# Kernel tuning notes

Measured on AMD Instinct MI355X. Metric: run time of the kernel, lower is better.

## Reference

```python
import jax, jax.numpy as jnp
import numpy as np

N = 100_000      # nodes
E = 1_600_000    # edges (before self loops)
IN = 128         # in_dim
HID = 64         # hidden_dim (per head)
HEADS = 2
NEG_SLOPE = 0.2  # PyG GATConv default negative_slope


def setup_inputs() -> dict:
    key = jax.random.key(0)
    k = jax.random.split(key, 6)
    x = jax.random.normal(k[0], (N, IN), jnp.float32)
    edge_index = jax.random.randint(k[1], (2, E), 0, N, dtype=jnp.int64)
    # GATConv linear (no bias in lin, bias added after aggregation in PyG)
    W = jax.random.normal(k[2], (IN, HEADS * HID), jnp.float32) * (1.0 / np.sqrt(IN))
    att_src = jax.random.normal(k[3], (HEADS, HID), jnp.float32) * 0.1
    att_dst = jax.random.normal(k[4], (HEADS, HID), jnp.float32) * 0.1
    bias = jnp.zeros((HEADS * HID,), jnp.float32)
    prelu_w = jnp.full((HEADS * HID,), 0.25, jnp.float32)  # nn.PReLU default init
    return {"x": x, "edge_index": edge_index, "W": W, "att_src": att_src,
            "att_dst": att_dst, "bias": bias, "prelu_w": prelu_w}


def reference(x, edge_index, W, att_src, att_dst, bias, prelu_w):
    n = x.shape[0]
    h = (x @ W).reshape(n, HEADS, HID)                 # [N,H,C]
    a_s = jnp.einsum('nhc,hc->nh', h, att_src)         # [N,H]
    a_d = jnp.einsum('nhc,hc->nh', h, att_dst)         # [N,H]
    # add self loops (PyG default add_self_loops=True)
    loops = jnp.arange(n, dtype=edge_index.dtype)
    src = jnp.concatenate([edge_index[0], loops])      # [Et]
    dst = jnp.concatenate([edge_index[1], loops])      # [Et]
    logits = a_s[src] + a_d[dst]                       # [Et,H]
    logits = jnp.where(logits >= 0, logits, NEG_SLOPE * logits)  # LeakyReLU
    # segment softmax over destination neighborhoods
    m = jax.ops.segment_max(logits, dst, num_segments=n)         # [N,H]
    e = jnp.exp(logits - m[dst])
    s = jax.ops.segment_sum(e, dst, num_segments=n)              # [N,H]
    alpha = e / (s[dst] + 1e-16)                                 # [Et,H]
    # (attention dropout p=0.2 is identity in eval mode)
    msg = h[src] * alpha[..., None]                    # [Et,H,C]
    out = jax.ops.segment_sum(msg, dst, num_segments=n).reshape(n, HEADS * HID)
    out = out + bias
    # PReLU with per-channel weight
    return jnp.where(out >= 0, out, prelu_w * out)
```

## Files before the change

### kernel.cpp

```cpp
#include <hip/hip_runtime.h>
#include <hip/hip_fp16.h>
#include <cstdint>
#include <cstddef>

#define NEG_SLOPE 0.2f
#define BSH 9
#define BNODES 512
#define CAP 12288

typedef __attribute__((ext_vector_type(8))) short short8v;
typedef __attribute__((ext_vector_type(4))) float f32x4;

__device__ __forceinline__ uint32_t bf16pair(float a, float b) {
    uint32_t ua = __float_as_uint(a), ub = __float_as_uint(b);
    ua = (ua + 0x7fffu + ((ua >> 16) & 1u)) >> 16;
    ub = (ub + 0x7fffu + ((ub >> 16) & 1u)) >> 16;
    return ua | (ub << 16);
}
__device__ __forceinline__ uint16_t rne16(float f) {
    uint32_t u = __float_as_uint(f);
    return (uint16_t)((u + 0x7fffu + ((u >> 16) & 1u)) >> 16);
}
__device__ __forceinline__ float bflo(uint32_t u) { return __uint_as_float(u << 16); }
__device__ __forceinline__ float bfhi(uint32_t u) { return __uint_as_float(u & 0xffff0000u); }
__device__ __forceinline__ uint32_t packf16(float a, float b) {
    __half2 h = __floats2half2_rn(a, b);
    return *reinterpret_cast<uint32_t*>(&h);
}

__global__ __launch_bounds__(256, 3) void gemm_att(
    const float* __restrict__ x, const float* __restrict__ W,
    const float* __restrict__ att_src, const float* __restrict__ att_dst,
    uint32_t* __restrict__ hb, float* __restrict__ a_s, float* __restrict__ a_d,
    int n)
{
    constexpr int PW = 136;
    __shared__ unsigned short Wt[128 * PW];
    __shared__ unsigned short Hs[4][16 * PW];
    const int tid  = threadIdx.x;
    const int w    = tid >> 6;
    const int lane = tid & 63;
    const int cl   = lane & 15;
    const int gq   = lane >> 4;
    const int base = blockIdx.x * 64;

    const float4* W4 = (const float4*)W;
#pragma unroll
    for (int i = 0; i < 16; ++i) {
        int idx = tid + i * 256;
        int k = idx >> 5, c0 = (idx & 31) * 4;
        float4 v = W4[idx];
        Wt[(c0 + 0) * PW + k] = rne16(v.x);
        Wt[(c0 + 1) * PW + k] = rne16(v.y);
        Wt[(c0 + 2) * PW + k] = rne16(v.z);
        Wt[(c0 + 3) * PW + k] = rne16(v.w);
    }

    float asr[8], adr[8];
#pragma unroll
    for (int t = 0; t < 8; ++t) {
        asr[t] = att_src[t * 16 + cl];
        adr[t] = att_dst[t * 16 + cl];
    }
    __syncthreads();

    const int rowg = base + w * 16 + cl;
    const int rowc = rowg < n ? rowg : (n - 1);
    const float4* xp = (const float4*)(x + (size_t)rowc * 128);

    f32x4 acc[8];
#pragma unroll
    for (int t = 0; t < 8; ++t) acc[t] = (f32x4){0.f, 0.f, 0.f, 0.f};

#pragma unroll
    for (int s = 0; s < 4; ++s) {
        int kq = s * 8 + gq * 2;
        float4 f0 = xp[kq], f1 = xp[kq + 1];
        union { short8v v; uint32_t d[4]; } A;
        A.d[0] = bf16pair(f0.x, f0.y);
        A.d[1] = bf16pair(f0.z, f0.w);
        A.d[2] = bf16pair(f1.x, f1.y);
        A.d[3] = bf16pair(f1.z, f1.w);
#pragma unroll
        for (int t = 0; t < 8; ++t) {
            union { short8v v; uint4 q; } B;
            B.q = *(const uint4*)&Wt[(t * 16 + cl) * PW + s * 32 + gq * 8];
            acc[t] = __builtin_amdgcn_mfma_f32_16x16x32_bf16(A.v, B.v, acc[t], 0, 0, 0);
        }
    }

    float ps0[4], ps1[4], pd0[4], pd1[4];
#pragma unroll
    for (int r = 0; r < 4; ++r) { ps0[r] = ps1[r] = pd0[r] = pd1[r] = 0.f; }
#pragma unroll
    for (int t = 0; t < 8; ++t) {
#pragma unroll
        for (int r = 0; r < 4; ++r) {
            float v = acc[t][r];
            if (t < 4) { ps0[r] = fmaf(v, asr[t], ps0[r]); pd0[r] = fmaf(v, adr[t], pd0[r]); }
            else       { ps1[r] = fmaf(v, asr[t], ps1[r]); pd1[r] = fmaf(v, adr[t], pd1[r]); }
        }
    }
#pragma unroll
    for (int off = 1; off < 16; off <<= 1) {
#pragma unroll
        for (int r = 0; r < 4; ++r) {
            ps0[r] += __shfl_xor(ps0[r], off);
            ps1[r] += __shfl_xor(ps1[r], off);
            pd0[r] += __shfl_xor(pd0[r], off);
            pd1[r] += __shfl_xor(pd1[r], off);
        }
    }
    if (cl == 0) {
#pragma unroll
        for (int r = 0; r < 4; ++r) {
            int rg = base + w * 16 + gq * 4 + r;
            if (rg < n) {
                a_s[rg * 2 + 0] = ps0[r]; a_s[rg * 2 + 1] = ps1[r];
                a_d[rg * 2 + 0] = pd0[r]; a_d[rg * 2 + 1] = pd1[r];
            }
        }
    }

#pragma unroll
    for (int t = 0; t < 8; ++t) {
#pragma unroll
        for (int r = 0; r < 4; ++r) {
            int row = gq * 4 + r;
            Hs[w][row * PW + t * 16 + cl] = rne16(acc[t][r]);
        }
    }
    __syncthreads();
#pragma unroll
    for (int q = 0; q < 4; ++q) {
        int row = q * 4 + gq;
        int cu  = 4 * cl;
        uint4 v = *(const uint4*)&Hs[w][row * PW + cu * 2];
        int rg = base + w * 16 + row;
        if (rg < n) *(uint4*)&hb[(size_t)rg * 64 + cu] = v;
    }
}

__global__ void zero_gcur(int* gcur, int nb) {
    if ((int)threadIdx.x < nb) gcur[threadIdx.x] = 0;
}

__global__ __launch_bounds__(256) void bucket_scatter(
    const int* __restrict__ src, const int* __restrict__ dst,
    int* __restrict__ gcur, uint32_t* __restrict__ pairs, int e, int nb)
{
    __shared__ int histL[256];
    __shared__ int gbaseL[256];
    const int tid = threadIdx.x;
    const int t0  = blockIdx.x * 4096;

    if (tid < nb) histL[tid] = 0;
    __syncthreads();

    int      myb[16];
    int      myslot[16];
    uint32_t mypk[16];
#pragma unroll 16
    for (int k = 0; k < 16; ++k) {
        int i = t0 + tid + k * 256;
        if (i < e) {
            int s = src[i], d = dst[i];
            int b = d >> BSH;
            myb[k]    = b;
            mypk[k]   = (uint32_t)s | ((uint32_t)(d & (BNODES - 1)) << 17);
            myslot[k] = atomicAdd(&histL[b], 1);
        } else myb[k] = -1;
    }
    __syncthreads();
    if (tid < nb) {
        int c = histL[tid];
        gbaseL[tid] = c ? atomicAdd(&gcur[tid], c) : 0;
    }
    __syncthreads();
#pragma unroll 16
    for (int k = 0; k < 16; ++k) {
        if (myb[k] >= 0) {
            int p = gbaseL[myb[k]] + myslot[k];
            if (p < CAP) pairs[(size_t)myb[k] * CAP + p] = mypk[k];
        }
    }
}

__global__ __launch_bounds__(256) void bucket_scan(
    const int* __restrict__ gcur, int* __restrict__ bbase, int* __restrict__ bcnt,
    int nb, int n)
{
    __shared__ int sh[256];
    const int tid = threadIdx.x;
    int nodes = 0, c = 0;
    if (tid < nb) {
        nodes = min(BNODES, n - tid * BNODES);
        c = min(gcur[tid], CAP);
    }
    int tot = c + nodes;
    sh[tid] = tot;
    __syncthreads();
    for (int off = 1; off < 256; off <<= 1) {
        int t = (tid >= off) ? sh[tid - off] : 0;
        __syncthreads();
        sh[tid] += t;
        __syncthreads();
    }
    if (tid < nb) { bbase[tid] = sh[tid] - tot; bcnt[tid] = c; }
}

__global__ __launch_bounds__(512) void build_csr(
    const uint32_t* __restrict__ pairs, const int* __restrict__ bbase,
    const int* __restrict__ bcnt, const float* __restrict__ a_s,
    const float* __restrict__ a_d,
    int* __restrict__ row_ptr, int* __restrict__ cnt, int* __restrict__ col,
    uint32_t* __restrict__ alph, float2* __restrict__ invs, int n)
{
    __shared__ uint32_t pl[CAP];
    __shared__ int degL[BNODES], curL[BNODES], scanL[BNODES];
    __shared__ float sumL[BNODES * 2];
    __shared__ float adL[BNODES * 2];
    const int b = blockIdx.x, tid = threadIdx.x;
    const int nbase = b * BNODES;
    const int nodes = min(BNODES, n - nbase);
    const int C     = bcnt[b];
    const int base  = bbase[b];

    degL[tid] = 1;
    float es0 = 0.f, es1 = 0.f;
    if (tid < nodes) {
        int g = nbase + tid;
        float2 ad = ((const float2*)a_d)[g];
        adL[2 * tid]     = ad.x;
        adL[2 * tid + 1] = ad.y;
        float2 as = ((const float2*)a_s)[g];
        float l0 = as.x + ad.x; l0 = l0 >= 0.f ? l0 : NEG_SLOPE * l0;
        float l1 = as.y + ad.y; l1 = l1 >= 0.f ? l1 : NEG_SLOPE * l1;
        es0 = __expf(l0); es1 = __expf(l1);
        sumL[2 * tid] = es0; sumL[2 * tid + 1] = es1;
    }
    __syncthreads();
    for (int i = tid; i < C; i += 512) {
        uint32_t p = pairs[(size_t)b * CAP + i];
        pl[i] = p;
        atomicAdd(&degL[p >> 17], 1);
    }
    __syncthreads();
    int v = (tid < nodes) ? degL[tid] : 0;
    scanL[tid] = v;
    __syncthreads();
    for (int off = 1; off < 512; off <<= 1) {
        int t = (tid >= off) ? scanL[tid - off] : 0;
        __syncthreads();
        scanL[tid] += t;
        __syncthreads();
    }
    if (tid < nodes) {
        int exc = scanL[tid] - v;
        int g   = nbase + tid;
        row_ptr[g] = base + exc;
        cnt[g]     = v;
        col[base + exc]  = g;
        alph[base + exc] = packf16(es0, es1);
        curL[tid]  = exc + 1;
    }
    __syncthreads();
    for (int i = tid; i < C; i += 512) {
        uint32_t p  = pl[i];
        int dl  = p >> 17;
        int s   = p & 0x1FFFF;
        float2 as = ((const float2*)a_s)[s];
        float l0 = as.x + adL[2 * dl];     l0 = l0 >= 0.f ? l0 : NEG_SLOPE * l0;
        float l1 = as.y + adL[2 * dl + 1]; l1 = l1 >= 0.f ? l1 : NEG_SLOPE * l1;
        float e0 = __expf(l0), e1 = __expf(l1);
        int pos = atomicAdd(&curL[dl], 1);
        col[base + pos]  = s;
        alph[base + pos] = packf16(e0, e1);
        atomicAdd(&sumL[2 * dl],     e0);
        atomicAdd(&sumL[2 * dl + 1], e1);
    }
    __syncthreads();
    if (tid < nodes) {
        float2 iv;
        iv.x = 1.f / (sumL[2 * tid]     + 1e-16f);
        iv.y = 1.f / (sumL[2 * tid + 1] + 1e-16f);
        invs[nbase + tid] = iv;
    }
}

__global__ __launch_bounds__(256) void attn_agg(
    const uint32_t* __restrict__ hb, const uint32_t* __restrict__ alph,
    const float2* __restrict__ invs, const int* __restrict__ row_ptr,
    const int* __restrict__ cnt, const int* __restrict__ col,
    const float* __restrict__ bias, const float* __restrict__ prelu_w,
    float* __restrict__ out, int n)
{
    const int gw   = (blockIdx.x * blockDim.x + threadIdx.x) >> 6;
    const int lane = threadIdx.x & 63;
    if (gw >= n) return;
    const int start = row_ptr[gw];
    const int deg   = cnt[gw];
    const float2 inv = invs[gw];

    if (deg <= 64) {
        int sv = 0; float al0 = 0.f, al1 = 0.f;
        if (lane < deg) {
            sv = col[start + lane];
            uint32_t ea = alph[start + lane];
            __half2 h2 = *reinterpret_cast<__half2*>(&ea);
            al0 = __half2float(__low2half(h2))  * inv.x;
            al1 = __half2float(__high2half(h2)) * inv.y;
        }
        const int g = lane >> 4, r = lane & 15;
        float acc[8];
#pragma unroll
        for (int q = 0; q < 8; ++q) acc[q] = 0.f;

        const uint4* hb4 = (const uint4*)hb;
        const int iters = (deg + 3) >> 2;
        for (int jj = 0; jj < iters; ++jj) {
            const int j = jj * 4 + g;
            int   s  = __shfl(sv, j);
            float A0 = __shfl(al0, j);
            float A1 = __shfl(al1, j);
            float A  = (r < 8) ? A0 : A1;
            if (j < deg) {
                uint4 q = hb4[(size_t)s * 16 + r];
                acc[0] = fmaf(A, bflo(q.x), acc[0]);
                acc[1] = fmaf(A, bfhi(q.x), acc[1]);
                acc[2] = fmaf(A, bflo(q.y), acc[2]);
                acc[3] = fmaf(A, bfhi(q.y), acc[3]);
                acc[4] = fmaf(A, bflo(q.z), acc[4]);
                acc[5] = fmaf(A, bfhi(q.z), acc[5]);
                acc[6] = fmaf(A, bflo(q.w), acc[6]);
                acc[7] = fmaf(A, bfhi(q.w), acc[7]);
            }
        }
#pragma unroll
        for (int q = 0; q < 8; ++q) {
            acc[q] += __shfl_xor(acc[q], 16);
            acc[q] += __shfl_xor(acc[q], 32);
        }
        if (lane < 16) {
            float4 b0 = ((const float4*)bias)[lane * 2];
            float4 b1 = ((const float4*)bias)[lane * 2 + 1];
            float4 p0 = ((const float4*)prelu_w)[lane * 2];
            float4 p1 = ((const float4*)prelu_w)[lane * 2 + 1];
            float4 w0, w1;
            w0.x = acc[0] + b0.x; w0.x = w0.x >= 0.f ? w0.x : p0.x * w0.x;
            w0.y = acc[1] + b0.y; w0.y = w0.y >= 0.f ? w0.y : p0.y * w0.y;
            w0.z = acc[2] + b0.z; w0.z = w0.z >= 0.f ? w0.z : p0.z * w0.z;
            w0.w = acc[3] + b0.w; w0.w = w0.w >= 0.f ? w0.w : p0.w * w0.w;
            w1.x = acc[4] + b1.x; w1.x = w1.x >= 0.f ? w1.x : p1.x * w1.x;
            w1.y = acc[5] + b1.y; w1.y = w1.y >= 0.f ? w1.y : p1.y * w1.y;
            w1.z = acc[6] + b1.z; w1.z = w1.z >= 0.f ? w1.z : p1.z * w1.z;
            w1.w = acc[7] + b1.w; w1.w = w1.w >= 0.f ? w1.w : p1.w * w1.w;
            ((float4*)out)[(size_t)gw * 32 + lane * 2]     = w0;
            ((float4*)out)[(size_t)gw * 32 + lane * 2 + 1] = w1;
        }
    } else {
        float accL = 0.f, accH = 0.f;
        for (int t0 = 0; t0 < deg; t0 += 64) {
            int tt = t0 + lane;
            int sv = 0; float al0 = 0.f, al1 = 0.f;
            if (tt < deg) {
                sv = col[start + tt];
                uint32_t ea = alph[start + tt];
                __half2 h2 = *reinterpret_cast<__half2*>(&ea);
                al0 = __half2float(__low2half(h2))  * inv.x;
                al1 = __half2float(__high2half(h2)) * inv.y;
            }
            int kmax = min(64, deg - t0);
            for (int j = 0; j < kmax; ++j) {
                int   s  = __shfl(sv, j);
                float A0 = __shfl(al0, j);
                float A1 = __shfl(al1, j);
                float A  = (lane < 32) ? A0 : A1;
                uint32_t u = hb[(size_t)s * 64 + lane];
                accL = fmaf(A, bflo(u), accL);
                accH = fmaf(A, bfhi(u), accH);
            }
        }
        float2 bz = ((const float2*)bias)[lane];
        float2 pw = ((const float2*)prelu_w)[lane];
        float o0 = accL + bz.x, o1 = accH + bz.y;
        o0 = o0 >= 0.f ? o0 : pw.x * o0;
        o1 = o1 >= 0.f ? o1 : pw.y * o1;
        float2 rr; rr.x = o0; rr.y = o1;
        ((float2*)out)[(size_t)gw * 64 + lane] = rr;
    }
}

extern "C" void kernel_launch(void* const* d_in, const int* in_sizes, int n_in,
                              void* d_out, int out_size, void* d_ws, size_t ws_size,
                              hipStream_t stream)
{
    const float* x        = (const float*)d_in[0];
    const int*   ei       = (const int*)d_in[1];
    const float* W        = (const float*)d_in[2];
    const float* att_src  = (const float*)d_in[3];
    const float* att_dst  = (const float*)d_in[4];
    const float* bias     = (const float*)d_in[5];
    const float* prelu_w  = (const float*)d_in[6];
    float* out = (float*)d_out;

    const int n = in_sizes[0] / 128;
    const int e = in_sizes[1] / 2;
    const int* srcp = ei;
    const int* dstp = ei + e;
    const int nb = (n + BNODES - 1) / BNODES;

    uint32_t* hb   = (uint32_t*)d_ws;
    float*    a_s  = (float*)(hb + (size_t)n * 64);
    float*    a_d  = a_s + (size_t)n * 2;
    float2*   invs = (float2*)(a_d + (size_t)n * 2);
    int*      gcur = (int*)(invs + n);
    int*      bbase= gcur + nb;
    int*      bcnt = bbase + nb;
    int*      row_ptr = bcnt + nb;
    int*      cnt  = row_ptr + n;
    uint32_t* pairs= (uint32_t*)(cnt + n);
    int*      col  = (int*)(pairs + (size_t)nb * CAP);
    uint32_t* alph = (uint32_t*)(col + (size_t)e + n);

    gemm_att<<<(n + 63) / 64, 256, 0, stream>>>(x, W, att_src, att_dst,
                                                hb, a_s, a_d, n);
    zero_gcur<<<1, 256, 0, stream>>>(gcur, nb);
    bucket_scatter<<<(e + 4095) / 4096, 256, 0, stream>>>(srcp, dstp, gcur, pairs, e, nb);
    bucket_scan<<<1, 256, 0, stream>>>(gcur, bbase, bcnt, nb, n);
    build_csr<<<nb, 512, 0, stream>>>(pairs, bbase, bcnt, a_s, a_d,
                                      row_ptr, cnt, col, alph, invs, n);
    attn_agg<<<(n + 3) / 4, 256, 0, stream>>>(hb, alph, invs, row_ptr, cnt, col,
                                              bias, prelu_w, out, n);
}
```

Measured before the change: 167.5 us.

## Fuse bucket scan and zeroing into neighbours, pack edge and node metadata

```diff
diff --git a/kernel.cpp b/kernel.cpp
--- a/kernel.cpp
+++ b/kernel.cpp
@@ -32,7 +32,7 @@
     const float* __restrict__ x, const float* __restrict__ W,
     const float* __restrict__ att_src, const float* __restrict__ att_dst,
     uint32_t* __restrict__ hb, float* __restrict__ a_s, float* __restrict__ a_d,
-    int n)
+    int* __restrict__ gcur, int nb, int n)
 {
     constexpr int PW = 136;
     __shared__ unsigned short Wt[128 * PW];
@@ -44,6 +44,8 @@
     const int gq   = lane >> 4;
     const int base = blockIdx.x * 64;
 
+    if (blockIdx.x == 0 && tid < nb) gcur[tid] = 0;
+
     const float4* W4 = (const float4*)W;
 #pragma unroll
     for (int i = 0; i < 16; ++i) {
@@ -139,10 +141,6 @@
         int rg = base + w * 16 + row;
         if (rg < n) *(uint4*)&hb[(size_t)rg * 64 + cu] = v;
     }
-}
-
-__global__ void zero_gcur(int* gcur, int nb) {
-    if ((int)threadIdx.x < nb) gcur[threadIdx.x] = 0;
 }
 
 __global__ __launch_bounds__(256) void bucket_scatter(
@@ -186,45 +184,40 @@
     }
 }
 
-__global__ __launch_bounds__(256) void bucket_scan(
-    const int* __restrict__ gcur, int* __restrict__ bbase, int* __restrict__ bcnt,
-    int nb, int n)
-{
-    __shared__ int sh[256];
-    const int tid = threadIdx.x;
-    int nodes = 0, c = 0;
-    if (tid < nb) {
-        nodes = min(BNODES, n - tid * BNODES);
-        c = min(gcur[tid], CAP);
-    }
-    int tot = c + nodes;
-    sh[tid] = tot;
-    __syncthreads();
-    for (int off = 1; off < 256; off <<= 1) {
-        int t = (tid >= off) ? sh[tid - off] : 0;
-        __syncthreads();
-        sh[tid] += t;
-        __syncthreads();
-    }
-    if (tid < nb) { bbase[tid] = sh[tid] - tot; bcnt[tid] = c; }
-}
-
-__global__ __launch_bounds__(512) void build_csr(
-    const uint32_t* __restrict__ pairs, const int* __restrict__ bbase,
-    const int* __restrict__ bcnt, const float* __restrict__ a_s,
-    const float* __restrict__ a_d,
-    int* __restrict__ row_ptr, int* __restrict__ cnt, int* __restrict__ col,
-    uint32_t* __restrict__ alph, float2* __restrict__ invs, int n)
+__global__ __launch_bounds__(512, 2) void build_csr(
+    const uint32_t* __restrict__ pairs, const int* __restrict__ gcur,
+    const float* __restrict__ a_s, const float* __restrict__ a_d,
+    uint4* __restrict__ meta, uint2* __restrict__ edges, int n, int nb)
 {
     __shared__ uint32_t pl[CAP];
-    __shared__ int degL[BNODES], curL[BNODES], scanL[BNODES];
+    __shared__ int degL[BNODES], curL[BNODES];
     __shared__ float sumL[BNODES * 2];
     __shared__ float adL[BNODES * 2];
+    __shared__ int bscan[256];
+    __shared__ int wsum[8];
     const int b = blockIdx.x, tid = threadIdx.x;
+    const int lane = tid & 63, wid = tid >> 6;
     const int nbase = b * BNODES;
     const int nodes = min(BNODES, n - nbase);
-    const int C     = bcnt[b];
-    const int base  = bbase[b];
+
+    if (tid < 256) {
+        int tot = 0;
+        if (tid < nb) {
+            int nn = min(BNODES, n - tid * BNODES);
+            tot = min(gcur[tid], CAP) + nn;
+        }
+        bscan[tid] = tot;
+    }
+    __syncthreads();
+    for (int off = 1; off < 256; off <<= 1) {
+        int t = 0;
+        if (tid < 256 && tid >= off) t = bscan[tid - off];
+        __syncthreads();
+        if (tid < 256) bscan[tid] += t;
+        __syncthreads();
+    }
+    const int C    = min(gcur[b], CAP);
+    const int base = bscan[b] - (C + nodes);
 
     degL[tid] = 1;
     float es0 = 0.f, es1 = 0.f;
@@ -246,23 +239,24 @@
         atomicAdd(&degL[p >> 17], 1);
     }
     __syncthreads();
+
     int v = (tid < nodes) ? degL[tid] : 0;
-    scanL[tid] = v;
-    __syncthreads();
-    for (int off = 1; off < 512; off <<= 1) {
-        int t = (tid >= off) ? scanL[tid - off] : 0;
-        __syncthreads();
-        scanL[tid] += t;
-        __syncthreads();
-    }
+    int sc = v;
+#pragma unroll
+    for (int off = 1; off < 64; off <<= 1) {
+        int t = __shfl_up(sc, off);
+        if (lane >= off) sc += t;
+    }
+    if (lane == 63) wsum[wid] = sc;
+    __syncthreads();
+    int woff = 0;
+#pragma unroll
+    for (int k = 0; k < 8; ++k) woff += (k < wid) ? wsum[k] : 0;
+    const int exc = sc - v + woff;
+
     if (tid < nodes) {
-        int exc = scanL[tid] - v;
-        int g   = nbase + tid;
-        row_ptr[g] = base + exc;
-        cnt[g]     = v;
-        col[base + exc]  = g;
-        alph[base + exc] = packf16(es0, es1);
-        curL[tid]  = exc + 1;
+        edges[base + exc] = make_uint2((uint32_t)(nbase + tid), packf16(es0, es1));
+        curL[tid] = exc + 1;
     }
     __syncthreads();
     for (int i = tid; i < C; i += 512) {
@@ -274,42 +268,44 @@
         float l1 = as.y + adL[2 * dl + 1]; l1 = l1 >= 0.f ? l1 : NEG_SLOPE * l1;
         float e0 = __expf(l0), e1 = __expf(l1);
         int pos = atomicAdd(&curL[dl], 1);
-        col[base + pos]  = s;
-        alph[base + pos] = packf16(e0, e1);
+        edges[base + pos] = make_uint2((uint32_t)s, packf16(e0, e1));
         atomicAdd(&sumL[2 * dl],     e0);
         atomicAdd(&sumL[2 * dl + 1], e1);
     }
     __syncthreads();
     if (tid < nodes) {
-        float2 iv;
-        iv.x = 1.f / (sumL[2 * tid]     + 1e-16f);
-        iv.y = 1.f / (sumL[2 * tid + 1] + 1e-16f);
-        invs[nbase + tid] = iv;
+        uint4 m;
+        m.x = (uint32_t)(base + exc);
+        m.y = (uint32_t)v;
+        m.z = __float_as_uint(1.f / (sumL[2 * tid]     + 1e-16f));
+        m.w = __float_as_uint(1.f / (sumL[2 * tid + 1] + 1e-16f));
+        meta[nbase + tid] = m;
     }
 }
 
 __global__ __launch_bounds__(256) void attn_agg(
-    const uint32_t* __restrict__ hb, const uint32_t* __restrict__ alph,
-    const float2* __restrict__ invs, const int* __restrict__ row_ptr,
-    const int* __restrict__ cnt, const int* __restrict__ col,
+    const uint32_t* __restrict__ hb, const uint2* __restrict__ edges,
+    const uint4* __restrict__ meta,
     const float* __restrict__ bias, const float* __restrict__ prelu_w,
     float* __restrict__ out, int n)
 {
     const int gw   = (blockIdx.x * blockDim.x + threadIdx.x) >> 6;
     const int lane = threadIdx.x & 63;
     if (gw >= n) return;
-    const int start = row_ptr[gw];
-    const int deg   = cnt[gw];
-    const float2 inv = invs[gw];
+    const uint4 mt  = meta[gw];
+    const int start = (int)mt.x;
+    const int deg   = (int)mt.y;
+    const float inv0 = __uint_as_float(mt.z);
+    const float inv1 = __uint_as_float(mt.w);
 
     if (deg <= 64) {
         int sv = 0; float al0 = 0.f, al1 = 0.f;
         if (lane < deg) {
-            sv = col[start + lane];
-            uint32_t ea = alph[start + lane];
-            __half2 h2 = *reinterpret_cast<__half2*>(&ea);
-            al0 = __half2float(__low2half(h2))  * inv.x;
-            al1 = __half2float(__high2half(h2)) * inv.y;
+            uint2 ed = edges[start + lane];
+            sv = (int)ed.x;
+            __half2 h2 = *reinterpret_cast<__half2*>(&ed.y);
+            al0 = __half2float(__low2half(h2))  * inv0;
+            al1 = __half2float(__high2half(h2)) * inv1;
         }
         const int g = lane >> 4, r = lane & 15;
         float acc[8];
@@ -317,24 +313,33 @@
         for (int q = 0; q < 8; ++q) acc[q] = 0.f;
 
         const uint4* hb4 = (const uint4*)hb;
-        const int iters = (deg + 3) >> 2;
+        const int iters = (deg + 7) >> 3;
         for (int jj = 0; jj < iters; ++jj) {
-            const int j = jj * 4 + g;
-            int   s  = __shfl(sv, j);
-            float A0 = __shfl(al0, j);
-            float A1 = __shfl(al1, j);
-            float A  = (r < 8) ? A0 : A1;
-            if (j < deg) {
-                uint4 q = hb4[(size_t)s * 16 + r];
-                acc[0] = fmaf(A, bflo(q.x), acc[0]);
-                acc[1] = fmaf(A, bfhi(q.x), acc[1]);
-                acc[2] = fmaf(A, bflo(q.y), acc[2]);
-                acc[3] = fmaf(A, bfhi(q.y), acc[3]);
-                acc[4] = fmaf(A, bflo(q.z), acc[4]);
-                acc[5] = fmaf(A, bfhi(q.z), acc[5]);
-                acc[6] = fmaf(A, bflo(q.w), acc[6]);
-                acc[7] = fmaf(A, bfhi(q.w), acc[7]);
-            }
+            const int ja = jj * 8 + g, jb = ja + 4;
+            int   sa  = __shfl(sv, ja);
+            int   sb  = __shfl(sv, jb);
+            float A0a = __shfl(al0, ja), A1a = __shfl(al1, ja);
+            float A0b = __shfl(al0, jb), A1b = __shfl(al1, jb);
+            float Aa  = (r < 8) ? A0a : A1a;
+            float Ab  = (r < 8) ? A0b : A1b;
+            uint4 qa = hb4[(size_t)sa * 16 + r];
+            uint4 qb = hb4[(size_t)sb * 16 + r];
+            acc[0] = fmaf(Aa, bflo(qa.x), acc[0]);
+            acc[1] = fmaf(Aa, bfhi(qa.x), acc[1]);
+            acc[2] = fmaf(Aa, bflo(qa.y), acc[2]);
+            acc[3] = fmaf(Aa, bfhi(qa.y), acc[3]);
+            acc[4] = fmaf(Aa, bflo(qa.z), acc[4]);
+            acc[5] = fmaf(Aa, bfhi(qa.z), acc[5]);
+            acc[6] = fmaf(Aa, bflo(qa.w), acc[6]);
+            acc[7] = fmaf(Aa, bfhi(qa.w), acc[7]);
+            acc[0] = fmaf(Ab, bflo(qb.x), acc[0]);
+            acc[1] = fmaf(Ab, bfhi(qb.x), acc[1]);
+            acc[2] = fmaf(Ab, bflo(qb.y), acc[2]);
+            acc[3] = fmaf(Ab, bfhi(qb.y), acc[3]);
+            acc[4] = fmaf(Ab, bflo(qb.z), acc[4]);
+            acc[5] = fmaf(Ab, bfhi(qb.z), acc[5]);
+            acc[6] = fmaf(Ab, bflo(qb.w), acc[6]);
+            acc[7] = fmaf(Ab, bfhi(qb.w), acc[7]);
         }
 #pragma unroll
         for (int q = 0; q < 8; ++q) {
@@ -364,11 +369,11 @@
             int tt = t0 + lane;
             int sv = 0; float al0 = 0.f, al1 = 0.f;
             if (tt < deg) {
-                sv = col[start + tt];
-                uint32_t ea = alph[start + tt];
-                __half2 h2 = *reinterpret_cast<__half2*>(&ea);
-                al0 = __half2float(__low2half(h2))  * inv.x;
-                al1 = __half2float(__high2half(h2)) * inv.y;
+                uint2 ed = edges[start + tt];
+                sv = (int)ed.x;
+                __half2 h2 = *reinterpret_cast<__half2*>(&ed.y);
+                al0 = __half2float(__low2half(h2))  * inv0;
+                al1 = __half2float(__high2half(h2)) * inv1;
             }
             int kmax = min(64, deg - t0);
             for (int j = 0; j < kmax; ++j) {
@@ -410,26 +415,17 @@
     const int* dstp = ei + e;
     const int nb = (n + BNODES - 1) / BNODES;
 
-    uint32_t* hb   = (uint32_t*)d_ws;
-    float*    a_s  = (float*)(hb + (size_t)n * 64);
-    float*    a_d  = a_s + (size_t)n * 2;
-    float2*   invs = (float2*)(a_d + (size_t)n * 2);
-    int*      gcur = (int*)(invs + n);
-    int*      bbase= gcur + nb;
-    int*      bcnt = bbase + nb;
-    int*      row_ptr = bcnt + nb;
-    int*      cnt  = row_ptr + n;
-    uint32_t* pairs= (uint32_t*)(cnt + n);
-    int*      col  = (int*)(pairs + (size_t)nb * CAP);
-    uint32_t* alph = (uint32_t*)(col + (size_t)e + n);
+    uint32_t* hb    = (uint32_t*)d_ws;
+    uint4*    meta  = (uint4*)(hb + (size_t)n * 64);
+    float*    a_s   = (float*)(meta + n);
+    float*    a_d   = a_s + (size_t)n * 2;
+    int*      gcur  = (int*)(a_d + (size_t)n * 2);
+    uint32_t* pairs = (uint32_t*)(gcur + 256);
+    uint2*    edges = (uint2*)(pairs + (size_t)nb * CAP);
 
     gemm_att<<<(n + 63) / 64, 256, 0, stream>>>(x, W, att_src, att_dst,
-                                                hb, a_s, a_d, n);
-    zero_gcur<<<1, 256, 0, stream>>>(gcur, nb);
+                                                hb, a_s, a_d, gcur, nb, n);
     bucket_scatter<<<(e + 4095) / 4096, 256, 0, stream>>>(srcp, dstp, gcur, pairs, e, nb);
-    bucket_scan<<<1, 256, 0, stream>>>(gcur, bbase, bcnt, nb, n);
-    build_csr<<<nb, 512, 0, stream>>>(pairs, bbase, bcnt, a_s, a_d,
-                                      row_ptr, cnt, col, alph, invs, n);
-    attn_agg<<<(n + 3) / 4, 256, 0, stream>>>(hb, alph, invs, row_ptr, cnt, col,
-                                              bias, prelu_w, out, n);
-}
+    build_csr<<<nb, 512, 0, stream>>>(pairs, gcur, a_s, a_d, meta, edges, n, nb);
+    attn_agg<<<(n + 3) / 4, 256, 0, stream>>>(hb, edges, meta, bias, prelu_w, out, n);
+}
```

New measurement: 158.9 us. -5.2%, faster.
